# Kernel tuning notes

Hardware: AMD Instinct MI355X
Metric: run time of the kernel (lower is better)

The kernel has to match this reference:

```python
import jax, jax.numpy as jnp
import numpy as np

N = 12288
E = 393216
H = 128
NEG = -1000000000.0

def setup_inputs() -> dict:
    key = jax.random.key(0)
    k1, k2, k3, k4, k5, k6 = jax.random.split(key, 6)
    h = jax.random.normal(k1, (N, H), dtype=jnp.float32)
    sources = jax.random.randint(k2, (E,), 0, N, dtype=jnp.int32)
    dests = jax.random.randint(k3, (E,), 0, N, dtype=jnp.int32)
    weights = jax.random.normal(k4, (E, 1), dtype=jnp.float32)
    # nn.Linear(2*H+1, 1) params
    W = jax.random.normal(k5, (1, 2 * H + 1), dtype=jnp.float32) / np.sqrt(2 * H + 1)
    b = jax.random.normal(k6, (1,), dtype=jnp.float32) * 0.01
    return {"h": h, "sources": sources, "dests": dests, "weights": weights, "W": W, "b": b}

def reference(h, sources, dests, weights, W, b):
    n = h.shape[0]
    # gather endpoint features and concat with edge weights: [E, 2H+1]
    edge_input = jnp.concatenate([h[dests], h[sources], weights], axis=1)
    vals = (edge_input @ W.T + b)[:, 0]  # [E]
    scores = jnp.full((n, n), NEG, dtype=h.dtype)
    scores = scores.at[dests, sources].set(vals)
    return scores
```

## Files before the change

### kernel.cpp

```cpp
#include <hip/hip_runtime.h>
#include <hip/hip_bf16.h>

#define NEG_VAL -1000000000.0f

__global__ void node_dots(const float* __restrict__ h,
                          const float* __restrict__ W,
                          float* __restrict__ a,
                          float* __restrict__ c,
                          int N) {
    int gid  = blockIdx.x * blockDim.x + threadIdx.x;
    int node = gid >> 6;
    int lane = threadIdx.x & 63;
    if (node >= N) return;

    const float2* h2 = (const float2*)(h + (size_t)node * 128);
    float2 v  = h2[lane];
    float2 wd = ((const float2*)W)[lane];
    float2 ws = ((const float2*)(W + 128))[lane];

    float sd = v.x * wd.x + v.y * wd.y;
    float ss = v.x * ws.x + v.y * ws.y;

    #pragma unroll
    for (int off = 32; off; off >>= 1) {
        sd += __shfl_xor(sd, off, 64);
        ss += __shfl_xor(ss, off, 64);
    }
    if (lane == 0) {
        a[node] = sd;
        c[node] = ss;
    }
}

__global__ void fill_neg(float4* __restrict__ out, long long n4) {
    long long i = (long long)blockIdx.x * blockDim.x + threadIdx.x;
    if (i < n4) {
        out[i] = make_float4(NEG_VAL, NEG_VAL, NEG_VAL, NEG_VAL);
    }
}

__global__ void edge_scatter(const int* __restrict__ src,
                             const int* __restrict__ dst,
                             const float* __restrict__ wgt,
                             const float* __restrict__ a,
                             const float* __restrict__ c,
                             const float* __restrict__ W,
                             const float* __restrict__ b,
                             float* __restrict__ out,
                             int E, int N) {
    int e = blockIdx.x * blockDim.x + threadIdx.x;
    if (e >= E) return;
    int s = src[e];
    int d = dst[e];
    float val = a[d] + c[s] + wgt[e] * W[256] + b[0];
    out[(size_t)d * N + s] = val;
}

extern "C" void kernel_launch(void* const* d_in, const int* in_sizes, int n_in,
                              void* d_out, int out_size, void* d_ws, size_t ws_size,
                              hipStream_t stream) {
    const float* h       = (const float*)d_in[0];
    const int*   sources = (const int*)d_in[1];
    const int*   dests   = (const int*)d_in[2];
    const float* weights = (const float*)d_in[3];
    const float* W       = (const float*)d_in[4];
    const float* b       = (const float*)d_in[5];
    float* out = (float*)d_out;

    const int N = in_sizes[0] / 128;
    const int E = in_sizes[1];

    float* a = (float*)d_ws;
    float* c = a + N;

    {
        int waves_per_block = 256 / 64;
        int blocks = (N + waves_per_block - 1) / waves_per_block;
        node_dots<<<blocks, 256, 0, stream>>>(h, W, a, c, N);
    }

    {
        long long n4 = (long long)out_size / 4;
        long long blocks = (n4 + 255) / 256;
        fill_neg<<<(int)blocks, 256, 0, stream>>>((float4*)out, n4);
    }

    {
        int blocks = (E + 255) / 256;
        edge_scatter<<<blocks, 256, 0, stream>>>(sources, dests, weights, a, c, W, b,
                                                 out, E, N);
    }
}
```

Measured before the change: 629.9 us.

## Fuse node dot products with grid-stride nontemporal fill into one launch

The node dot-product kernel and the fill of the output matrix with the negative constant are merged into one launch, with block ranges assigned to each role. The fill now uses a grid-stride loop over a fixed set of 4096 blocks and nontemporal vector stores, replacing one thread per float4. The aim is to cut a kernel launch, spread the 600MB fill over persistent blocks, and keep the streaming writes from polluting cache. The nontemporal stores may delay the scatter kernel's later writes landing in the same lines, and the edge value is now computed with an FMA, which changes rounding slightly.

After: 674.3 us. +7.1%, slower.

```diff
diff --git a/kernel.cpp b/kernel.cpp
--- a/kernel.cpp
+++ b/kernel.cpp
@@ -1,58 +1,69 @@
 #include <hip/hip_runtime.h>
-#include <hip/hip_bf16.h>
 
 #define NEG_VAL -1000000000.0f
 
-__global__ void node_dots(const float* __restrict__ h,
-                          const float* __restrict__ W,
-                          float* __restrict__ a,
-                          float* __restrict__ c,
-                          int N) {
-    int gid  = blockIdx.x * blockDim.x + threadIdx.x;
-    int node = gid >> 6;
-    int lane = threadIdx.x & 63;
-    if (node >= N) return;
+typedef float v4f __attribute__((ext_vector_type(4)));
 
-    const float2* h2 = (const float2*)(h + (size_t)node * 128);
-    float2 v  = h2[lane];
-    float2 wd = ((const float2*)W)[lane];
-    float2 ws = ((const float2*)(W + 128))[lane];
+__global__ __launch_bounds__(256) void dots_and_fill(
+    const float* __restrict__ h,
+    const float* __restrict__ W,
+    float* __restrict__ a,
+    float* __restrict__ c,
+    int N,
+    v4f* __restrict__ out4,
+    long long n4,
+    int dotBlocks,
+    int fillBlocks)
+{
+    if ((int)blockIdx.x < dotBlocks) {
+        int gid  = blockIdx.x * 256 + threadIdx.x;
+        int node = gid >> 6;
+        int lane = threadIdx.x & 63;
+        if (node >= N) return;
 
-    float sd = v.x * wd.x + v.y * wd.y;
-    float ss = v.x * ws.x + v.y * ws.y;
+        const float2* h2 = (const float2*)(h + (size_t)node * 128);
+        float2 v  = h2[lane];
+        float2 wd = ((const float2*)W)[lane];
+        float2 ws = ((const float2*)(W + 128))[lane];
 
-    #pragma unroll
-    for (int off = 32; off; off >>= 1) {
-        sd += __shfl_xor(sd, off, 64);
-        ss += __shfl_xor(ss, off, 64);
-    }
-    if (lane == 0) {
-        a[node] = sd;
-        c[node] = ss;
+        float sd = v.x * wd.x + v.y * wd.y;
+        float ss = v.x * ws.x + v.y * ws.y;
+
+        #pragma unroll
+        for (int off = 32; off; off >>= 1) {
+            sd += __shfl_xor(sd, off, 64);
+            ss += __shfl_xor(ss, off, 64);
+        }
+        if (lane == 0) {
+            a[node] = sd;
+            c[node] = ss;
+        }
+    } else {
+        long long tid    = (long long)(blockIdx.x - dotBlocks) * 256 + threadIdx.x;
+        long long stride = (long long)fillBlocks * 256;
+        const v4f v = { NEG_VAL, NEG_VAL, NEG_VAL, NEG_VAL };
+        for (long long i = tid; i < n4; i += stride) {
+            __builtin_nontemporal_store(v, out4 + i);
+        }
     }
 }
 
-__global__ void fill_neg(float4* __restrict__ out, long long n4) {
-    long long i = (long long)blockIdx.x * blockDim.x + threadIdx.x;
-    if (i < n4) {
-        out[i] = make_float4(NEG_VAL, NEG_VAL, NEG_VAL, NEG_VAL);
-    }
-}
-
-__global__ void edge_scatter(const int* __restrict__ src,
-                             const int* __restrict__ dst,
-                             const float* __restrict__ wgt,
-                             const float* __restrict__ a,
-                             const float* __restrict__ c,
-                             const float* __restrict__ W,
-                             const float* __restrict__ b,
-                             float* __restrict__ out,
-                             int E, int N) {
+__global__ __launch_bounds__(256) void edge_scatter(
+    const int* __restrict__ src,
+    const int* __restrict__ dst,
+    const float* __restrict__ wgt,
+    const float* __restrict__ a,
+    const float* __restrict__ c,
+    const float* __restrict__ W,
+    const float* __restrict__ b,
+    float* __restrict__ out,
+    int E, int N)
+{
     int e = blockIdx.x * blockDim.x + threadIdx.x;
     if (e >= E) return;
     int s = src[e];
     int d = dst[e];
-    float val = a[d] + c[s] + wgt[e] * W[256] + b[0];
+    float val = fmaf(wgt[e], W[256], a[d] + c[s] + b[0]);
     out[(size_t)d * N + s] = val;
 }
 
@@ -74,15 +85,11 @@
     float* c = a + N;
 
     {
-        int waves_per_block = 256 / 64;
-        int blocks = (N + waves_per_block - 1) / waves_per_block;
-        node_dots<<<blocks, 256, 0, stream>>>(h, W, a, c, N);
-    }
-
-    {
+        int dotBlocks  = (N + 3) / 4;
+        int fillBlocks = 4096;
         long long n4 = (long long)out_size / 4;
-        long long blocks = (n4 + 255) / 256;
-        fill_neg<<<(int)blocks, 256, 0, stream>>>((float4*)out, n4);
+        dots_and_fill<<<dotBlocks + fillBlocks, 256, 0, stream>>>(
+            h, W, a, c, N, (v4f*)out, n4, dotBlocks, fillBlocks);
     }
 
     {
```
